# Optimization experiments

Hardware: AMD Instinct MI355X
Metric: run time of the kernel (lower is better)

Reference implementation:

```python
import jax, jax.numpy as jnp
import numpy as np

N_UE = 16384
N_AP = 128
E = 2097152
D = 32

relu = jax.nn.relu


def setup_inputs():
    key = jax.random.key(0)
    ks = jax.random.split(key, 24)
    def g(i, shape, s=0.1):
        return jax.random.normal(ks[i], shape, dtype=jnp.float32) * s
    inp = {}
    inp["x_ue"] = jax.random.uniform(ks[0], (N_UE, 1), dtype=jnp.float32)
    inp["e_ua"] = g(1, (E, 2), 1.0)
    inp["e_au"] = g(2, (E, 2), 1.0)
    inp["src"] = jax.random.randint(ks[3], (E,), 0, N_UE)
    inp["dst"] = jax.random.randint(ks[4], (E,), 0, N_AP)
    # layer 1 (Ue2Ap): ue feat dim 1, ap feat dim 0, edge dim 2
    inp["Wm1_ua"] = g(5, (1 + 2, D)); inp["bm1_ua"] = jnp.zeros((D,), jnp.float32)
    inp["Wm1_au"] = g(6, (2, D));     inp["bm1_au"] = jnp.zeros((D,), jnp.float32)
    inp["Wu1_ap"] = g(7, (D, D));     inp["bu1_ap"] = jnp.zeros((D,), jnp.float32)
    inp["Wu1_ue"] = g(8, (1 + D, D)); inp["bu1_ue"] = jnp.zeros((D,), jnp.float32)
    inp["We1_ua"] = g(9, (2 * D + 2, 2));  inp["be1_ua"] = jnp.zeros((2,), jnp.float32)
    inp["We1_au"] = g(10, (2 * D + 2, 2)); inp["be1_au"] = jnp.zeros((2,), jnp.float32)
    # layers 2-4 stacked (all 32 -> 32)
    inp["Wm_ua"] = g(11, (3, D + 2, D)); inp["bm_ua"] = jnp.zeros((3, D), jnp.float32)
    inp["Wm_au"] = g(12, (3, D + 2, D)); inp["bm_au"] = jnp.zeros((3, D), jnp.float32)
    inp["Wu_ap"] = g(13, (3, 2 * D, D)); inp["bu_ap"] = jnp.zeros((3, D), jnp.float32)
    inp["Wu_ue"] = g(14, (3, 2 * D, D)); inp["bu_ue"] = jnp.zeros((3, D), jnp.float32)
    inp["We_ua"] = g(15, (3, 2 * D + 2, 2)); inp["be_ua"] = jnp.zeros((3, 2), jnp.float32)
    inp["We_au"] = g(16, (3, 2 * D + 2, 2)); inp["be_au"] = jnp.zeros((3, 2), jnp.float32)
    # power head: mlp([32,16]) + Lin(16,1) + Sigmoid
    inp["Wp1"] = g(17, (D, 16)); inp["bp1"] = jnp.zeros((16,), jnp.float32)
    inp["Wp2"] = g(18, (16, 1)); inp["bp2"] = jnp.zeros((1,), jnp.float32)
    return inp


def _het_conv(x_ue, x_ap, e_ua, e_au, src, dst,
              Wm_ua, bm_ua, Wm_au, bm_au,
              Wu_ap, bu_ap, Wu_ue, bu_ue,
              We_ua, be_ua, We_au, be_au):
    # ue -> ap: gather src ue feats + edge attr, MLP, scatter-add to ap
    f_ua = jnp.concatenate([x_ue[src], e_ua], axis=1)        # [E, d_ue+2]
    m_ua = relu(f_ua @ Wm_ua + bm_ua)                        # [E, D]
    agg_ap = jax.ops.segment_sum(m_ua, dst, num_segments=N_AP)
    # ap -> ue: ap has no features in layer 1 (dim 0)
    f_au = e_au if x_ap is None else jnp.concatenate([x_ap[dst], e_au], axis=1)
    m_au = relu(f_au @ Wm_au + bm_au)                        # [E, D]
    agg_ue = jax.ops.segment_sum(m_au, src, num_segments=N_UE)
    # node updates
    h_ap = agg_ap if x_ap is None else jnp.concatenate([x_ap, agg_ap], axis=1)
    x_ap_new = relu(h_ap @ Wu_ap + bu_ap)                    # [N_AP, D]
    x_ue_new = relu(jnp.concatenate([x_ue, agg_ue], axis=1) @ Wu_ue + bu_ue)  # [N_UE, D]
    # edge updates (keep edge_dim = 2)
    pair = jnp.concatenate([x_ue_new[src], x_ap_new[dst]], axis=1)  # [E, 2D]
    e_ua_new = relu(jnp.concatenate([pair, e_ua], axis=1) @ We_ua + be_ua)
    e_au_new = relu(jnp.concatenate([pair, e_au], axis=1) @ We_au + be_au)
    return x_ue_new, x_ap_new, e_ua_new, e_au_new


def reference(x_ue, e_ua, e_au, src, dst,
              Wm1_ua, bm1_ua, Wm1_au, bm1_au, Wu1_ap, bu1_ap, Wu1_ue, bu1_ue,
              We1_ua, be1_ua, We1_au, be1_au,
              Wm_ua, bm_ua, Wm_au, bm_au, Wu_ap, bu_ap, Wu_ue, bu_ue,
              We_ua, be_ua, We_au, be_au,
              Wp1, bp1, Wp2, bp2):
    x_ue, x_ap, e_ua, e_au = _het_conv(
        x_ue, None, e_ua, e_au, src, dst,
        Wm1_ua, bm1_ua, Wm1_au, bm1_au, Wu1_ap, bu1_ap, Wu1_ue, bu1_ue,
        We1_ua, be1_ua, We1_au, be1_au)
    for l in range(3):  # conv2, conv3, conv4
        x_ue, x_ap, e_ua, e_au = _het_conv(
            x_ue, x_ap, e_ua, e_au, src, dst,
            Wm_ua[l], bm_ua[l], Wm_au[l], bm_au[l],
            Wu_ap[l], bu_ap[l], Wu_ue[l], bu_ue[l],
            We_ua[l], be_ua[l], We_au[l], be_au[l])
    power = jax.nn.sigmoid(relu(x_ue @ Wp1 + bp1) @ Wp2 + bp2)  # [N_UE, 1]
    ue_out = jnp.concatenate([x_ue[:, :1], power], axis=1)      # [N_UE, 2]
    return ue_out, x_ap, e_ua, e_au
```

## Files before the change

### kernel.cpp

```cpp
#include <hip/hip_runtime.h>
#include <math.h>

#define N_UE 16384
#define N_AP 128
#define NE   2097152
#define NSB  256
#define EPSB (NE / NSB)
#define APCH 128
#define NPART (N_AP * APCH)

__global__ __launch_bounds__(256) void init_kernel(
    const float* __restrict__ x_ue, const float* __restrict__ Wm1_ua,
    const float* __restrict__ bm1_ua, const float* __restrict__ bm1_au,
    float* __restrict__ Qua, float* __restrict__ Pau)
{
    int i = blockIdx.x * 256 + threadIdx.x;
    int d = i & 31;
    Qua[i] = fmaf(x_ue[i >> 5], Wm1_ua[d], bm1_ua[d]);
    if (i < N_AP * 32) Pau[i] = bm1_au[d];
}

__global__ __launch_bounds__(256) void hist_src(
    const int* __restrict__ src, int* __restrict__ histS)
{
    __shared__ int h[N_UE];
    for (int i = threadIdx.x; i < N_UE; i += 256) h[i] = 0;
    __syncthreads();
    const int beg = blockIdx.x * EPSB;
    for (int e = beg + threadIdx.x; e < beg + EPSB; e += 256)
        atomicAdd(&h[src[e]], 1);
    __syncthreads();
    for (int i = threadIdx.x; i < N_UE; i += 256) histS[blockIdx.x * N_UE + i] = h[i];
}

__global__ __launch_bounds__(256) void colscan_kernel(
    const int* __restrict__ histS, int* __restrict__ baseS, int* __restrict__ cnt)
{
    const int u = blockIdx.x * 256 + threadIdx.x;
    int run = 0;
    for (int b = 0; b < NSB; ++b) {
        int t = histS[b * N_UE + u];
        baseS[b * N_UE + u] = run;
        run += t;
    }
    cnt[u] = run;
}

__global__ __launch_bounds__(256) void scan_kernel(
    const int* __restrict__ cnt, int* __restrict__ offs)
{
    __shared__ int ps[256];
    __shared__ int ps2[257];
    const int t = threadIdx.x;
    const int b0 = t * (N_UE / 256);
    int s = 0;
    for (int i = 0; i < N_UE / 256; ++i) s += cnt[b0 + i];
    ps[t] = s;
    __syncthreads();
    if (t == 0) {
        int r = 0;
        for (int i = 0; i < 256; ++i) { ps2[i] = r; r += ps[i]; }
        ps2[256] = r;
    }
    __syncthreads();
    int r = ps2[t];
    for (int i = 0; i < N_UE / 256; ++i) { offs[b0 + i] = r; r += cnt[b0 + i]; }
    if (t == 255) offs[N_UE] = ps2[256];
}

__global__ __launch_bounds__(256) void scatter_src(
    const int* __restrict__ src, const int* __restrict__ dst,
    const float2* __restrict__ e0au,
    const int* __restrict__ baseS, const int* __restrict__ offs,
    int* __restrict__ dtS, float2* __restrict__ attS, int* __restrict__ invS)
{
    __shared__ int cursor[N_UE];
    const int b = blockIdx.x;
    for (int i = threadIdx.x; i < N_UE; i += 256)
        cursor[i] = offs[i] + baseS[b * N_UE + i];
    __syncthreads();
    const int beg = b * EPSB;
    for (int e = beg + threadIdx.x; e < beg + EPSB; e += 256) {
        int s = src[e];
        int pos = atomicAdd(&cursor[s], 1);
        dtS[pos] = dst[e];
        attS[pos] = e0au[e];
        invS[e] = pos;
    }
}

__global__ __launch_bounds__(256) void hist_dst(
    const int* __restrict__ dst, int* __restrict__ histD)
{
    __shared__ int h[N_AP];
    if (threadIdx.x < N_AP) h[threadIdx.x] = 0;
    __syncthreads();
    const int beg = blockIdx.x * EPSB;
    for (int e = beg + threadIdx.x; e < beg + EPSB; e += 256)
        atomicAdd(&h[dst[e]], 1);
    __syncthreads();
    if (threadIdx.x < N_AP) histD[blockIdx.x * N_AP + threadIdx.x] = h[threadIdx.x];
}

__global__ __launch_bounds__(128) void scan_dst(
    const int* __restrict__ histD, int* __restrict__ offsD, int* __restrict__ offsDnode)
{
    __shared__ int colTot[N_AP], colStart[N_AP];
    const int a = threadIdx.x;
    int run = 0;
    for (int b = 0; b < NSB; ++b) {
        offsD[b * N_AP + a] = run;
        run += histD[b * N_AP + a];
    }
    colTot[a] = run;
    __syncthreads();
    if (a == 0) {
        int r = 0;
        for (int i = 0; i < N_AP; ++i) { colStart[i] = r; r += colTot[i]; }
    }
    __syncthreads();
    const int st = colStart[a];
    offsDnode[a] = st;
    if (a == 0) offsDnode[N_AP] = NE;
    for (int b = 0; b < NSB; ++b) offsD[b * N_AP + a] += st;
}

__global__ __launch_bounds__(256) void scatter_dst(
    const int* __restrict__ src, const int* __restrict__ dst,
    const float2* __restrict__ e0ua, const int* __restrict__ offsD,
    int* __restrict__ srcD, float2* __restrict__ attD, int* __restrict__ invD)
{
    __shared__ int cursor[N_AP];
    const int b = blockIdx.x;
    if (threadIdx.x < N_AP) cursor[threadIdx.x] = offsD[b * N_AP + threadIdx.x];
    __syncthreads();
    const int beg = b * EPSB;
    for (int e = beg + threadIdx.x; e < beg + EPSB; e += 256) {
        int dt = dst[e];
        int pos = atomicAdd(&cursor[dt], 1);
        srcD[pos] = src[e];
        attD[pos] = e0ua[e];
        invD[e] = pos;
    }
}

template<bool EUPD>
__global__ __launch_bounds__(256) void ue_pass(
    const int* __restrict__ offs, const int* __restrict__ dtS,
    const float2* __restrict__ attIn, float2* __restrict__ attOut,
    const float2* __restrict__ RueB, const float2* __restrict__ RapB,
    const float* __restrict__ EcB,
    const float* __restrict__ Pau, const float* __restrict__ cw,
    float* __restrict__ agg_ue)
{
    const int tid = threadIdx.x;
    const int u   = blockIdx.x * 8 + (tid >> 5);
    const int dim = tid & 31;

    const float w0 = cw[dim], w1 = cw[32 + dim];
    float d00 = 0.f, d01 = 0.f, d10 = 0.f, d11 = 0.f, rbx = 0.f, rby = 0.f;
    if constexpr (EUPD) {
        d00 = EcB[0]; d01 = EcB[1]; d10 = EcB[2]; d11 = EcB[3];
        float2 r = RueB[u]; rbx = r.x; rby = r.y;
    }

    const int e0 = offs[u], e1 = offs[u + 1];
    float acc = 0.f;
    #pragma unroll 4
    for (int e = e0; e < e1; ++e) {
        int dt = dtS[e];
        float2 ea = attIn[e];
        if constexpr (EUPD) {
            float2 rp = RapB[dt];
            float m0 = fmaxf(rbx + rp.x + ea.x * d00 + ea.y * d10, 0.f);
            float m1 = fmaxf(rby + rp.y + ea.x * d01 + ea.y * d11, 0.f);
            ea = make_float2(m0, m1);
            if (dim == 0) attOut[e] = ea;
        }
        float p = Pau[dt * 32 + dim];
        acc += fmaxf(fmaf(ea.x, w0, fmaf(ea.y, w1, p)), 0.f);
    }
    agg_ue[u * 32 + dim] = acc;
}

template<bool EUPD>
__global__ __launch_bounds__(256) void ap_pass(
    const int* __restrict__ offsDnode, const int* __restrict__ srcD,
    const float2* __restrict__ attIn, float2* __restrict__ attOut,
    const float2* __restrict__ RueA, const float2* __restrict__ RapA,
    const float* __restrict__ EcA,
    const float* __restrict__ Qua, const float* __restrict__ cu,
    float* __restrict__ partial)
{
    const int tid = threadIdx.x;
    const int gid = blockIdx.x * 8 + (tid >> 5);
    const int dim = tid & 31;
    const int a   = gid >> 7;
    const int c   = gid & 127;

    const float u0 = cu[dim], u1 = cu[32 + dim];
    float c00 = 0.f, c01 = 0.f, c10 = 0.f, c11 = 0.f, rax = 0.f, ray = 0.f;
    if constexpr (EUPD) {
        c00 = EcA[0]; c01 = EcA[1]; c10 = EcA[2]; c11 = EcA[3];
        float2 r = RapA[a]; rax = r.x; ray = r.y;
    }

    const int s0 = offsDnode[a], s1 = offsDnode[a + 1];
    const int len = s1 - s0;
    const int b0 = s0 + (int)(((long long)len * c) >> 7);
    const int b1 = s0 + (int)(((long long)len * (c + 1)) >> 7);

    float acc = 0.f;
    #pragma unroll 4
    for (int e = b0; e < b1; ++e) {
        int s = srcD[e];
        float2 ea = attIn[e];
        if constexpr (EUPD) {
            float2 ru = RueA[s];
            float n0 = fmaxf(rax + ru.x + ea.x * c00 + ea.y * c10, 0.f);
            float n1 = fmaxf(ray + ru.y + ea.x * c01 + ea.y * c11, 0.f);
            ea = make_float2(n0, n1);
            if (dim == 0) attOut[e] = ea;
        }
        float q = Qua[s * 32 + dim];
        acc += fmaxf(fmaf(ea.x, u0, fmaf(ea.y, u1, q)), 0.f);
    }
    partial[gid * 32 + dim] = acc;
}

__global__ __launch_bounds__(256) void final_edge(
    const int* __restrict__ src, const int* __restrict__ dst,
    const int* __restrict__ invS, const int* __restrict__ invD,
    const float2* __restrict__ attS, const float2* __restrict__ attD,
    const float2* __restrict__ RueA, const float2* __restrict__ RueB,
    const float2* __restrict__ RapA, const float2* __restrict__ RapB,
    const float* __restrict__ EcA, const float* __restrict__ EcB,
    float2* __restrict__ out_eua, float2* __restrict__ out_eau)
{
    const int e = blockIdx.x * 256 + threadIdx.x;
    const int s = src[e], dt = dst[e];
    float c00 = EcA[0], c01 = EcA[1], c10 = EcA[2], c11 = EcA[3];
    float d00 = EcB[0], d01 = EcB[1], d10 = EcB[2], d11 = EcB[3];
    float2 eua = attD[invD[e]];
    float2 eau = attS[invS[e]];
    float2 rA = RueA[s], pA = RapA[dt];
    float n0 = fmaxf(rA.x + pA.x + eua.x * c00 + eua.y * c10, 0.f);
    float n1 = fmaxf(rA.y + pA.y + eua.x * c01 + eua.y * c11, 0.f);
    float2 rB = RueB[s], pB = RapB[dt];
    float m0 = fmaxf(rB.x + pB.x + eau.x * d00 + eau.y * d10, 0.f);
    float m1 = fmaxf(rB.y + pB.y + eau.x * d01 + eau.y * d11, 0.f);
    out_eua[e] = make_float2(n0, n1);
    out_eau[e] = make_float2(m0, m1);
}

template<bool FIRST, bool LAST>
__global__ __launch_bounds__(256) void node_ue_kernel(
    const float* __restrict__ x_prev, const float* __restrict__ agg_ue,
    const float* __restrict__ Wu, const float* __restrict__ bu,
    const float* __restrict__ Wm_next, const float* __restrict__ bm_next,
    const float* __restrict__ WeUa, const float* __restrict__ WeUb,
    const float* __restrict__ Wp1, const float* __restrict__ bp1,
    const float* __restrict__ Wp2, const float* __restrict__ bp2,
    float* __restrict__ x_new, float* __restrict__ Qua_next,
    float2* __restrict__ RueA, float2* __restrict__ RueB,
    float2* __restrict__ ue_out)
{
    constexpr int KIN = FIRST ? 33 : 64;
    __shared__ float Wu_s[64 * 32];
    __shared__ float Wm_s[32 * 32];
    __shared__ float WeA_s[64], WeB_s[64];
    __shared__ float bu_s[32], bm_s[32];
    __shared__ float Wp1_s[32 * 16], bp1_s[16], Wp2_s[16];

    const int tid = threadIdx.x;
    for (int i = tid; i < KIN * 32; i += 256) Wu_s[i] = Wu[i];
    if (tid < 32) bu_s[tid] = bu[tid];
    if (!LAST) {
        for (int i = tid; i < 1024; i += 256) Wm_s[i] = Wm_next[i];
        if (tid < 32) bm_s[tid] = bm_next[tid];
    }
    if (tid < 64) { WeA_s[tid] = WeUa[tid]; WeB_s[tid] = WeUb[tid]; }
    if (LAST) {
        for (int i = tid; i < 512; i += 256) Wp1_s[i] = Wp1[i];
        if (tid < 16) { bp1_s[tid] = bp1[tid]; Wp2_s[tid] = Wp2[tid]; }
    }
    __syncthreads();

    const int u = blockIdx.x * 256 + tid;
    float in[KIN];
    if (FIRST) {
        in[0] = x_prev[u];
        #pragma unroll
        for (int k = 0; k < 32; ++k) in[1 + k] = agg_ue[u * 32 + k];
    } else {
        #pragma unroll
        for (int k = 0; k < 32; ++k) in[k] = x_prev[u * 32 + k];
        #pragma unroll
        for (int k = 0; k < 32; ++k) in[32 + k] = agg_ue[u * 32 + k];
    }
    float out[32];
    #pragma unroll
    for (int d = 0; d < 32; ++d) {
        float acc = bu_s[d];
        #pragma unroll
        for (int k = 0; k < KIN; ++k) acc = fmaf(in[k], Wu_s[k * 32 + d], acc);
        out[d] = fmaxf(acc, 0.f);
    }
    #pragma unroll
    for (int d = 0; d < 32; ++d) x_new[u * 32 + d] = out[d];
    if (!LAST) {
        #pragma unroll
        for (int d = 0; d < 32; ++d) {
            float acc = bm_s[d];
            #pragma unroll
            for (int k = 0; k < 32; ++k) acc = fmaf(out[k], Wm_s[k * 32 + d], acc);
            Qua_next[u * 32 + d] = acc;
        }
    }
    float r0 = 0.f, r1 = 0.f, s0 = 0.f, s1 = 0.f;
    #pragma unroll
    for (int k = 0; k < 32; ++k) {
        r0 = fmaf(out[k], WeA_s[k * 2],     r0);
        r1 = fmaf(out[k], WeA_s[k * 2 + 1], r1);
        s0 = fmaf(out[k], WeB_s[k * 2],     s0);
        s1 = fmaf(out[k], WeB_s[k * 2 + 1], s1);
    }
    RueA[u] = make_float2(r0, r1);
    RueB[u] = make_float2(s0, s1);
    if (LAST) {
        float z = bp2[0];
        #pragma unroll
        for (int j = 0; j < 16; ++j) {
            float h = bp1_s[j];
            #pragma unroll
            for (int k = 0; k < 32; ++k) h = fmaf(out[k], Wp1_s[k * 16 + j], h);
            z = fmaf(fmaxf(h, 0.f), Wp2_s[j], z);
        }
        float pw = 1.f / (1.f + expf(-z));
        ue_out[u] = make_float2(out[0], pw);
    }
}

template<bool FIRST, bool LAST>
__global__ __launch_bounds__(256) void node_ap_kernel(
    const float* __restrict__ partial,
    const float* __restrict__ x_prev,
    const float* __restrict__ Wu, const float* __restrict__ bu,
    const float* __restrict__ Wm_next, const float* __restrict__ bm_next,
    const float* __restrict__ WeA, const float* __restrict__ beA,
    const float* __restrict__ WeB, const float* __restrict__ beB,
    float* __restrict__ x_new, float* __restrict__ Pau_next,
    float2* __restrict__ RapA, float2* __restrict__ RapB)
{
    __shared__ float red[256];
    __shared__ float agg_s[32];
    __shared__ float xnew_s[32];
    const int a = blockIdx.x, tid = threadIdx.x;
    const int d = tid & 31, p0 = tid >> 5;
    float acc = 0.f;
    for (int p = p0; p < APCH; p += 8)
        acc += partial[(size_t)(a * APCH + p) * 32 + d];
    red[tid] = acc;
    __syncthreads();
    if (tid < 32) {
        float s = 0.f;
        #pragma unroll
        for (int i = 0; i < 8; ++i) s += red[i * 32 + tid];
        agg_s[tid] = s;
    }
    __syncthreads();
    if (tid < 32) {
        float acc2 = bu[d];
        if (FIRST) {
            #pragma unroll
            for (int k = 0; k < 32; ++k) acc2 = fmaf(agg_s[k], Wu[k * 32 + d], acc2);
        } else {
            #pragma unroll
            for (int k = 0; k < 32; ++k) acc2 = fmaf(x_prev[a * 32 + k], Wu[k * 32 + d], acc2);
            #pragma unroll
            for (int k = 0; k < 32; ++k) acc2 = fmaf(agg_s[k], Wu[(32 + k) * 32 + d], acc2);
        }
        float xn = fmaxf(acc2, 0.f);
        xnew_s[d] = xn;
        x_new[a * 32 + d] = xn;
    }
    __syncthreads();
    if (!LAST) {
        if (tid < 32) {
            float acc3 = bm_next[d];
            #pragma unroll
            for (int k = 0; k < 32; ++k) acc3 = fmaf(xnew_s[k], Wm_next[k * 32 + d], acc3);
            Pau_next[a * 32 + d] = acc3;
        }
    }
    if (tid == 0) {
        float q0 = beA[0], q1 = beA[1], t0 = beB[0], t1 = beB[1];
        #pragma unroll
        for (int k = 0; k < 32; ++k) {
            q0 = fmaf(xnew_s[k], WeA[k * 2],     q0);
            q1 = fmaf(xnew_s[k], WeA[k * 2 + 1], q1);
            t0 = fmaf(xnew_s[k], WeB[k * 2],     t0);
            t1 = fmaf(xnew_s[k], WeB[k * 2 + 1], t1);
        }
        RapA[a] = make_float2(q0, q1);
        RapB[a] = make_float2(t0, t1);
    }
}

extern "C" void kernel_launch(void* const* d_in, const int* in_sizes, int n_in,
                              void* d_out_v, int out_size, void* d_ws, size_t ws_size,
                              hipStream_t stream)
{
    const float*  x_ue   = (const float*)d_in[0];
    const float2* e0ua   = (const float2*)d_in[1];
    const float2* e0au   = (const float2*)d_in[2];
    const int*    src    = (const int*)d_in[3];
    const int*    dst    = (const int*)d_in[4];
    const float* Wm1_ua = (const float*)d_in[5];
    const float* bm1_ua = (const float*)d_in[6];
    const float* Wm1_au = (const float*)d_in[7];
    const float* bm1_au = (const float*)d_in[8];
    const float* Wu1_ap = (const float*)d_in[9];
    const float* bu1_ap = (const float*)d_in[10];
    const float* Wu1_ue = (const float*)d_in[11];
    const float* bu1_ue = (const float*)d_in[12];
    const float* We1_ua = (const float*)d_in[13];
    const float* be1_ua = (const float*)d_in[14];
    const float* We1_au = (const float*)d_in[15];
    const float* be1_au = (const float*)d_in[16];
    const float* Wm_ua  = (const float*)d_in[17];
    const float* bm_ua  = (const float*)d_in[18];
    const float* Wm_au  = (const float*)d_in[19];
    const float* bm_au  = (const float*)d_in[20];
    const float* Wu_ap  = (const float*)d_in[21];
    const float* bu_ap  = (const float*)d_in[22];
    const float* Wu_ue  = (const float*)d_in[23];
    const float* bu_ue  = (const float*)d_in[24];
    const float* We_ua  = (const float*)d_in[25];
    const float* be_ua  = (const float*)d_in[26];
    const float* We_au  = (const float*)d_in[27];
    const float* be_au  = (const float*)d_in[28];
    const float* Wp1    = (const float*)d_in[29];
    const float* bp1    = (const float*)d_in[30];
    const float* Wp2    = (const float*)d_in[31];
    const float* bp2    = (const float*)d_in[32];

    float*  outp    = (float*)d_out_v;
    float2* out_ue  = (float2*)outp;
    float*  out_ap  = outp + N_UE * 2;
    float2* out_eua = (float2*)(outp + N_UE * 2 + N_AP * 32);
    float2* out_eau = (float2*)(outp + N_UE * 2 + N_AP * 32 + (size_t)NE * 2);

    float* ws = (float*)d_ws;
    float* x_ueA  = ws;          ws += N_UE * 32;
    float* x_ueB  = ws;          ws += N_UE * 32;
    float* x_apA  = ws;          ws += N_AP * 32;
    float* x_apB  = ws;          ws += N_AP * 32;
    float* agg_ue = ws;          ws += N_UE * 32;
    float* Qua    = ws;          ws += N_UE * 32;
    float* Pau    = ws;          ws += N_AP * 32;
    float2* RueA  = (float2*)ws; ws += N_UE * 2;
    float2* RueB  = (float2*)ws; ws += N_UE * 2;
    float2* RapA  = (float2*)ws; ws += N_AP * 2;
    float2* RapB  = (float2*)ws; ws += N_AP * 2;
    float* partial = ws;         ws += (size_t)NPART * 32;
    int* cnt   = (int*)ws;       ws += N_UE;
    int* offs  = (int*)ws;       ws += N_UE + 4;
    int* histD = (int*)ws;       ws += NSB * N_AP;
    int* offsD = (int*)ws;       ws += NSB * N_AP;
    int* offsDnode = (int*)ws;   ws += N_AP + 4;
    int* invS  = (int*)ws;       ws += NE;
    int* invD  = (int*)ws;       ws += NE;
    int* dtS   = (int*)ws;       ws += NE;
    int* srcD  = (int*)ws;       ws += NE;
    float2* attS_A = (float2*)ws; ws += (size_t)NE * 2;
    float2* attS_B = (float2*)ws; ws += (size_t)NE * 2;
    float2* attD_A = (float2*)ws; ws += (size_t)NE * 2;
    float2* attD_B = (float2*)ws; ws += (size_t)NE * 2;
    int* histS = (int*)attS_B;
    int* baseS = (int*)attD_B;

    dim3 blk(256);

    hist_src<<<NSB, blk, 0, stream>>>(src, histS);
    colscan_kernel<<<N_UE / 256, blk, 0, stream>>>(histS, baseS, cnt);
    scan_kernel<<<1, blk, 0, stream>>>(cnt, offs);
    scatter_src<<<NSB, blk, 0, stream>>>(src, dst, e0au, baseS, offs, dtS, attS_A, invS);
    hist_dst<<<NSB, blk, 0, stream>>>(dst, histD);
    scan_dst<<<1, dim3(128), 0, stream>>>(histD, offsD, offsDnode);
    scatter_dst<<<NSB, blk, 0, stream>>>(src, dst, e0ua, offsD, srcD, attD_A, invD);

    init_kernel<<<N_UE * 32 / 256, blk, 0, stream>>>(x_ue, Wm1_ua, bm1_ua, bm1_au, Qua, Pau);

    ue_pass<false><<<N_UE / 8, blk, 0, stream>>>(
        offs, dtS, attS_A, nullptr, nullptr, nullptr, nullptr,
        Pau, Wm1_au, agg_ue);
    ap_pass<false><<<NPART / 8, blk, 0, stream>>>(
        offsDnode, srcD, attD_A, nullptr, nullptr, nullptr, nullptr,
        Qua, Wm1_ua + 32, partial);
    node_ue_kernel<true, false><<<N_UE / 256, blk, 0, stream>>>(
        x_ue, agg_ue, Wu1_ue, bu1_ue, Wm_ua, bm_ua, We1_ua, We1_au,
        nullptr, nullptr, nullptr, nullptr,
        x_ueA, Qua, RueA, RueB, nullptr);
    node_ap_kernel<true, false><<<N_AP, blk, 0, stream>>>(
        partial, nullptr, Wu1_ap, bu1_ap, Wm_au, bm_au,
        We1_ua + 64, be1_ua, We1_au + 64, be1_au,
        x_apA, Pau, RapA, RapB);

    ue_pass<true><<<N_UE / 8, blk, 0, stream>>>(
        offs, dtS, attS_A, attS_B, RueB, RapB, We1_au + 128,
        Pau, Wm_au + 1024, agg_ue);
    ap_pass<true><<<NPART / 8, blk, 0, stream>>>(
        offsDnode, srcD, attD_A, attD_B, RueA, RapA, We1_ua + 128,
        Qua, Wm_ua + 1024, partial);
    node_ue_kernel<false, false><<<N_UE / 256, blk, 0, stream>>>(
        x_ueA, agg_ue, Wu_ue, bu_ue, Wm_ua + 1088, bm_ua + 32, We_ua, We_au,
        nullptr, nullptr, nullptr, nullptr,
        x_ueB, Qua, RueA, RueB, nullptr);
    node_ap_kernel<false, false><<<N_AP, blk, 0, stream>>>(
        partial, x_apA, Wu_ap, bu_ap, Wm_au + 1088, bm_au + 32,
        We_ua + 64, be_ua, We_au + 64, be_au,
        x_apB, Pau, RapA, RapB);

    ue_pass<true><<<N_UE / 8, blk, 0, stream>>>(
        offs, dtS, attS_B, attS_A, RueB, RapB, We_au + 128,
        Pau, Wm_au + 2112, agg_ue);
    ap_pass<true><<<NPART / 8, blk, 0, stream>>>(
        offsDnode, srcD, attD_B, attD_A, RueA, RapA, We_ua + 128,
        Qua, Wm_ua + 2112, partial);
    node_ue_kernel<false, false><<<N_UE / 256, blk, 0, stream>>>(
        x_ueB, agg_ue, Wu_ue + 2048, bu_ue + 32, Wm_ua + 2176, bm_ua + 64,
        We_ua + 132, We_au + 132,
        nullptr, nullptr, nullptr, nullptr,
        x_ueA, Qua, RueA, RueB, nullptr);
    node_ap_kernel<false, false><<<N_AP, blk, 0, stream>>>(
        partial, x_apB, Wu_ap + 2048, bu_ap + 32, Wm_au + 2176, bm_au + 64,
        We_ua + 196, be_ua + 2, We_au + 196, be_au + 2,
        x_apA, Pau, RapA, RapB);

    ue_pass<true><<<N_UE / 8, blk, 0, stream>>>(
        offs, dtS, attS_A, attS_B, RueB, RapB, We_au + 260,
        Pau, Wm_au + 3200, agg_ue);
    ap_pass<true><<<NPART / 8, blk, 0, stream>>>(
        offsDnode, srcD, attD_A, attD_B, RueA, RapA, We_ua + 260,
        Qua, Wm_ua + 3200, partial);
    node_ue_kernel<false, true><<<N_UE / 256, blk, 0, stream>>>(
        x_ueA, agg_ue, Wu_ue + 4096, bu_ue + 64, nullptr, nullptr,
        We_ua + 264, We_au + 264,
        Wp1, bp1, Wp2, bp2,
        x_ueB, nullptr, RueA, RueB, out_ue);
    node_ap_kernel<false, true><<<N_AP, blk, 0, stream>>>(
        partial, x_apA, Wu_ap + 4096, bu_ap + 64, nullptr, nullptr,
        We_ua + 328, be_ua + 4, We_au + 328, be_au + 4,
        out_ap, nullptr, RapA, RapB);

    final_edge<<<NE / 256, blk, 0, stream>>>(
        src, dst, invS, invD, attS_B, attD_B,
        RueA, RueB, RapA, RapB,
        We_ua + 392, We_au + 392, out_eua, out_eau);
}
```

Baseline: 1.106 ms.

## Process edges in padded fixed-size chunks per thread with all 32 dims

Replaces the warp-per-node, lane-per-dimension edge passes with a thread-per-chunk scheme. Each node's edge list is padded to multiples of 8 (UE side) or 16 (AP side), using sentinel indices whose feature rows are -1e30 so the ReLU turns padding into zero. Each thread accumulates all 32 dimensions with float4 loads and writes a per-chunk partial, which a separate reduce kernel (or the AP node kernel) sums per node. Edge attributes are now updated in place rather than ping-ponged between two buffers. This aims to remove load imbalance and redundant per-lane index and attribute loads, at the cost of high register use per thread, extra partial-buffer traffic, and one extra reduction launch per layer.

```diff
diff --git a/kernel.cpp b/kernel.cpp
--- a/kernel.cpp
+++ b/kernel.cpp
@@ -6,8 +6,26 @@
 #define NE   2097152
 #define NSB  256
 #define EPSB (NE / NSB)
-#define APCH 128
-#define NPART (N_AP * APCH)
+#define CHS  8
+#define CHD  16
+#define NEP  (NE + CHS * N_UE)
+#define NCHU (NEP / CHS)
+#define NEPD (NE + CHD * N_AP)
+#define NCHD (NEPD / CHD)
+#define NCHD_AL 131328
+
+#define RFL(x) __int_as_float(__builtin_amdgcn_readfirstlane(__float_as_int(x)))
+
+__global__ __launch_bounds__(256) void prefill(
+    int* __restrict__ dtS, int* __restrict__ srcD,
+    int* __restrict__ cnS, int* __restrict__ cnD)
+{
+    int i = blockIdx.x * 256 + threadIdx.x;
+    dtS[i] = N_AP;
+    if (i < NEPD) srcD[i] = N_UE;
+    if (i < NCHU) cnS[i] = -1;
+    if (i < NCHD_AL) cnD[i] = -1;
+}
 
 __global__ __launch_bounds__(256) void init_kernel(
     const float* __restrict__ x_ue, const float* __restrict__ Wm1_ua,
@@ -18,6 +36,7 @@
     int d = i & 31;
     Qua[i] = fmaf(x_ue[i >> 5], Wm1_ua[d], bm1_ua[d]);
     if (i < N_AP * 32) Pau[i] = bm1_au[d];
+    if (i < 32) { Qua[N_UE * 32 + i] = -1e30f; Pau[N_AP * 32 + i] = -1e30f; }
 }
 
 __global__ __launch_bounds__(256) void hist_src(
@@ -46,15 +65,15 @@
     cnt[u] = run;
 }
 
-__global__ __launch_bounds__(256) void scan_kernel(
-    const int* __restrict__ cnt, int* __restrict__ offs)
+__global__ __launch_bounds__(256) void scan_src(
+    const int* __restrict__ cnt, int* __restrict__ CU)
 {
     __shared__ int ps[256];
     __shared__ int ps2[257];
     const int t = threadIdx.x;
     const int b0 = t * (N_UE / 256);
     int s = 0;
-    for (int i = 0; i < N_UE / 256; ++i) s += cnt[b0 + i];
+    for (int i = 0; i < N_UE / 256; ++i) s += (cnt[b0 + i] + CHS - 1) / CHS;
     ps[t] = s;
     __syncthreads();
     if (t == 0) {
@@ -64,20 +83,20 @@
     }
     __syncthreads();
     int r = ps2[t];
-    for (int i = 0; i < N_UE / 256; ++i) { offs[b0 + i] = r; r += cnt[b0 + i]; }
-    if (t == 255) offs[N_UE] = ps2[256];
+    for (int i = 0; i < N_UE / 256; ++i) { CU[b0 + i] = r; r += (cnt[b0 + i] + CHS - 1) / CHS; }
+    if (t == 255) CU[N_UE] = ps2[256];
 }
 
 __global__ __launch_bounds__(256) void scatter_src(
     const int* __restrict__ src, const int* __restrict__ dst,
     const float2* __restrict__ e0au,
-    const int* __restrict__ baseS, const int* __restrict__ offs,
+    const int* __restrict__ baseS, const int* __restrict__ CU,
     int* __restrict__ dtS, float2* __restrict__ attS, int* __restrict__ invS)
 {
     __shared__ int cursor[N_UE];
     const int b = blockIdx.x;
     for (int i = threadIdx.x; i < N_UE; i += 256)
-        cursor[i] = offs[i] + baseS[b * N_UE + i];
+        cursor[i] = CU[i] * CHS + baseS[b * N_UE + i];
     __syncthreads();
     const int beg = b * EPSB;
     for (int e = beg + threadIdx.x; e < beg + EPSB; e += 256) {
@@ -103,7 +122,7 @@
 }
 
 __global__ __launch_bounds__(128) void scan_dst(
-    const int* __restrict__ histD, int* __restrict__ offsD, int* __restrict__ offsDnode)
+    const int* __restrict__ histD, int* __restrict__ offsD, int* __restrict__ CA)
 {
     __shared__ int colTot[N_AP], colStart[N_AP];
     const int a = threadIdx.x;
@@ -116,12 +135,15 @@
     __syncthreads();
     if (a == 0) {
         int r = 0;
-        for (int i = 0; i < N_AP; ++i) { colStart[i] = r; r += colTot[i]; }
+        for (int i = 0; i < N_AP; ++i) {
+            CA[i] = r;
+            colStart[i] = r * CHD;
+            r += (colTot[i] + CHD - 1) / CHD;
+        }
+        CA[N_AP] = r;
     }
     __syncthreads();
     const int st = colStart[a];
-    offsDnode[a] = st;
-    if (a == 0) offsDnode[N_AP] = NE;
     for (int b = 0; b < NSB; ++b) offsD[b * N_AP + a] += st;
 }
 
@@ -144,88 +166,134 @@
     }
 }
 
+__global__ __launch_bounds__(256) void build_map_src(
+    const int* __restrict__ CU, int* __restrict__ cnS)
+{
+    const int u = blockIdx.x * 256 + threadIdx.x;
+    const int c0 = CU[u], c1 = CU[u + 1];
+    for (int c = c0; c < c1; ++c) cnS[c] = u;
+}
+
+__global__ __launch_bounds__(128) void build_map_dst(
+    const int* __restrict__ CA, int* __restrict__ cnD)
+{
+    const int a = threadIdx.x;
+    const int c0 = CA[a], c1 = CA[a + 1];
+    for (int c = c0; c < c1; ++c) cnD[c] = a;
+}
+
 template<bool EUPD>
-__global__ __launch_bounds__(256) void ue_pass(
-    const int* __restrict__ offs, const int* __restrict__ dtS,
-    const float2* __restrict__ attIn, float2* __restrict__ attOut,
+__global__ __launch_bounds__(256) void pass_src(
+    const int* __restrict__ cnS, const int* __restrict__ dtS,
+    float2* __restrict__ attS,
     const float2* __restrict__ RueB, const float2* __restrict__ RapB,
     const float* __restrict__ EcB,
     const float* __restrict__ Pau, const float* __restrict__ cw,
-    float* __restrict__ agg_ue)
-{
-    const int tid = threadIdx.x;
-    const int u   = blockIdx.x * 8 + (tid >> 5);
-    const int dim = tid & 31;
-
-    const float w0 = cw[dim], w1 = cw[32 + dim];
+    float* __restrict__ partialU)
+{
+    const int ch = blockIdx.x * 256 + threadIdx.x;
+    const int u = cnS[ch];
+    if (u < 0) return;
+    float w0v[32], w1v[32];
+    #pragma unroll
+    for (int d = 0; d < 32; ++d) { w0v[d] = RFL(cw[d]); w1v[d] = RFL(cw[32 + d]); }
     float d00 = 0.f, d01 = 0.f, d10 = 0.f, d11 = 0.f, rbx = 0.f, rby = 0.f;
     if constexpr (EUPD) {
-        d00 = EcB[0]; d01 = EcB[1]; d10 = EcB[2]; d11 = EcB[3];
+        d00 = RFL(EcB[0]); d01 = RFL(EcB[1]); d10 = RFL(EcB[2]); d11 = RFL(EcB[3]);
         float2 r = RueB[u]; rbx = r.x; rby = r.y;
     }
-
-    const int e0 = offs[u], e1 = offs[u + 1];
-    float acc = 0.f;
-    #pragma unroll 4
-    for (int e = e0; e < e1; ++e) {
-        int dt = dtS[e];
-        float2 ea = attIn[e];
+    const float4* __restrict__ Pau4 = (const float4*)Pau;
+    const int base = ch * CHS;
+    float4 acc[8];
+    #pragma unroll
+    for (int q = 0; q < 8; ++q) acc[q] = make_float4(0.f, 0.f, 0.f, 0.f);
+    #pragma unroll
+    for (int j = 0; j < CHS; ++j) {
+        int dt = dtS[base + j];
+        float2 a = attS[base + j];
         if constexpr (EUPD) {
             float2 rp = RapB[dt];
-            float m0 = fmaxf(rbx + rp.x + ea.x * d00 + ea.y * d10, 0.f);
-            float m1 = fmaxf(rby + rp.y + ea.x * d01 + ea.y * d11, 0.f);
-            ea = make_float2(m0, m1);
-            if (dim == 0) attOut[e] = ea;
-        }
-        float p = Pau[dt * 32 + dim];
-        acc += fmaxf(fmaf(ea.x, w0, fmaf(ea.y, w1, p)), 0.f);
-    }
-    agg_ue[u * 32 + dim] = acc;
+            float m0 = fmaxf(rbx + rp.x + a.x * d00 + a.y * d10, 0.f);
+            float m1 = fmaxf(rby + rp.y + a.x * d01 + a.y * d11, 0.f);
+            a = make_float2(m0, m1);
+            attS[base + j] = a;
+        }
+        const float4* pr = Pau4 + dt * 8;
+        #pragma unroll
+        for (int q = 0; q < 8; ++q) {
+            float4 pv = pr[q];
+            acc[q].x += fmaxf(fmaf(a.x, w0v[q*4+0], fmaf(a.y, w1v[q*4+0], pv.x)), 0.f);
+            acc[q].y += fmaxf(fmaf(a.x, w0v[q*4+1], fmaf(a.y, w1v[q*4+1], pv.y)), 0.f);
+            acc[q].z += fmaxf(fmaf(a.x, w0v[q*4+2], fmaf(a.y, w1v[q*4+2], pv.z)), 0.f);
+            acc[q].w += fmaxf(fmaf(a.x, w0v[q*4+3], fmaf(a.y, w1v[q*4+3], pv.w)), 0.f);
+        }
+    }
+    float4* pu = (float4*)(partialU + (size_t)ch * 32);
+    #pragma unroll
+    for (int q = 0; q < 8; ++q) pu[q] = acc[q];
 }
 
 template<bool EUPD>
-__global__ __launch_bounds__(256) void ap_pass(
-    const int* __restrict__ offsDnode, const int* __restrict__ srcD,
-    const float2* __restrict__ attIn, float2* __restrict__ attOut,
+__global__ __launch_bounds__(256) void pass_dst(
+    const int* __restrict__ cnD, const int* __restrict__ srcD,
+    float2* __restrict__ attD,
     const float2* __restrict__ RueA, const float2* __restrict__ RapA,
     const float* __restrict__ EcA,
     const float* __restrict__ Qua, const float* __restrict__ cu,
-    float* __restrict__ partial)
-{
-    const int tid = threadIdx.x;
-    const int gid = blockIdx.x * 8 + (tid >> 5);
-    const int dim = tid & 31;
-    const int a   = gid >> 7;
-    const int c   = gid & 127;
-
-    const float u0 = cu[dim], u1 = cu[32 + dim];
+    float* __restrict__ partialA)
+{
+    const int ch = blockIdx.x * 256 + threadIdx.x;
+    const int a = cnD[ch];
+    if (a < 0) return;
+    float u0v[32], u1v[32];
+    #pragma unroll
+    for (int d = 0; d < 32; ++d) { u0v[d] = RFL(cu[d]); u1v[d] = RFL(cu[32 + d]); }
     float c00 = 0.f, c01 = 0.f, c10 = 0.f, c11 = 0.f, rax = 0.f, ray = 0.f;
     if constexpr (EUPD) {
-        c00 = EcA[0]; c01 = EcA[1]; c10 = EcA[2]; c11 = EcA[3];
+        c00 = RFL(EcA[0]); c01 = RFL(EcA[1]); c10 = RFL(EcA[2]); c11 = RFL(EcA[3]);
         float2 r = RapA[a]; rax = r.x; ray = r.y;
     }
-
-    const int s0 = offsDnode[a], s1 = offsDnode[a + 1];
-    const int len = s1 - s0;
-    const int b0 = s0 + (int)(((long long)len * c) >> 7);
-    const int b1 = s0 + (int)(((long long)len * (c + 1)) >> 7);
-
-    float acc = 0.f;
+    const float4* __restrict__ Qua4 = (const float4*)Qua;
+    const int base = ch * CHD;
+    float4 acc[8];
+    #pragma unroll
+    for (int q = 0; q < 8; ++q) acc[q] = make_float4(0.f, 0.f, 0.f, 0.f);
     #pragma unroll 4
-    for (int e = b0; e < b1; ++e) {
-        int s = srcD[e];
-        float2 ea = attIn[e];
+    for (int j = 0; j < CHD; ++j) {
+        int s = srcD[base + j];
+        float2 a2 = attD[base + j];
         if constexpr (EUPD) {
             float2 ru = RueA[s];
-            float n0 = fmaxf(rax + ru.x + ea.x * c00 + ea.y * c10, 0.f);
-            float n1 = fmaxf(ray + ru.y + ea.x * c01 + ea.y * c11, 0.f);
-            ea = make_float2(n0, n1);
-            if (dim == 0) attOut[e] = ea;
-        }
-        float q = Qua[s * 32 + dim];
-        acc += fmaxf(fmaf(ea.x, u0, fmaf(ea.y, u1, q)), 0.f);
-    }
-    partial[gid * 32 + dim] = acc;
+            float n0 = fmaxf(rax + ru.x + a2.x * c00 + a2.y * c10, 0.f);
+            float n1 = fmaxf(ray + ru.y + a2.x * c01 + a2.y * c11, 0.f);
+            a2 = make_float2(n0, n1);
+            attD[base + j] = a2;
+        }
+        const float4* qr = Qua4 + s * 8;
+        #pragma unroll
+        for (int q = 0; q < 8; ++q) {
+            float4 qv = qr[q];
+            acc[q].x += fmaxf(fmaf(a2.x, u0v[q*4+0], fmaf(a2.y, u1v[q*4+0], qv.x)), 0.f);
+            acc[q].y += fmaxf(fmaf(a2.x, u0v[q*4+1], fmaf(a2.y, u1v[q*4+1], qv.y)), 0.f);
+            acc[q].z += fmaxf(fmaf(a2.x, u0v[q*4+2], fmaf(a2.y, u1v[q*4+2], qv.z)), 0.f);
+            acc[q].w += fmaxf(fmaf(a2.x, u0v[q*4+3], fmaf(a2.y, u1v[q*4+3], qv.w)), 0.f);
+        }
+    }
+    float4* pa = (float4*)(partialA + (size_t)ch * 32);
+    #pragma unroll
+    for (int q = 0; q < 8; ++q) pa[q] = acc[q];
+}
+
+__global__ __launch_bounds__(256) void reduce_ue(
+    const int* __restrict__ CU, const float* __restrict__ partialU,
+    float* __restrict__ agg_ue)
+{
+    const int g   = (blockIdx.x * 256 + threadIdx.x) >> 5;
+    const int dim = threadIdx.x & 31;
+    const int c0 = CU[g], c1 = CU[g + 1];
+    float acc = 0.f;
+    for (int c = c0; c < c1; ++c) acc += partialU[(size_t)c * 32 + dim];
+    agg_ue[g * 32 + dim] = acc;
 }
 
 __global__ __launch_bounds__(256) void final_edge(
@@ -343,7 +411,7 @@
 
 template<bool FIRST, bool LAST>
 __global__ __launch_bounds__(256) void node_ap_kernel(
-    const float* __restrict__ partial,
+    const float* __restrict__ partialA, const int* __restrict__ CA,
     const float* __restrict__ x_prev,
     const float* __restrict__ Wu, const float* __restrict__ bu,
     const float* __restrict__ Wm_next, const float* __restrict__ bm_next,
@@ -357,9 +425,10 @@
     __shared__ float xnew_s[32];
     const int a = blockIdx.x, tid = threadIdx.x;
     const int d = tid & 31, p0 = tid >> 5;
+    const int c0 = CA[a], c1 = CA[a + 1];
     float acc = 0.f;
-    for (int p = p0; p < APCH; p += 8)
-        acc += partial[(size_t)(a * APCH + p) * 32 + d];
+    for (int p = c0 + p0; p < c1; p += 8)
+        acc += partialA[(size_t)p * 32 + d];
     red[tid] = acc;
     __syncthreads();
     if (tid < 32) {
@@ -457,105 +526,105 @@
     float* x_apA  = ws;          ws += N_AP * 32;
     float* x_apB  = ws;          ws += N_AP * 32;
     float* agg_ue = ws;          ws += N_UE * 32;
-    float* Qua    = ws;          ws += N_UE * 32;
-    float* Pau    = ws;          ws += N_AP * 32;
-    float2* RueA  = (float2*)ws; ws += N_UE * 2;
-    float2* RueB  = (float2*)ws; ws += N_UE * 2;
-    float2* RapA  = (float2*)ws; ws += N_AP * 2;
-    float2* RapB  = (float2*)ws; ws += N_AP * 2;
-    float* partial = ws;         ws += (size_t)NPART * 32;
+    float* Qua    = ws;          ws += (N_UE + 1) * 32;
+    float* Pau    = ws;          ws += (N_AP + 1) * 32;
+    float2* RueA  = (float2*)ws; ws += (N_UE + 2) * 2;
+    float2* RueB  = (float2*)ws; ws += (N_UE + 2) * 2;
+    float2* RapA  = (float2*)ws; ws += (N_AP + 2) * 2;
+    float2* RapB  = (float2*)ws; ws += (N_AP + 2) * 2;
     int* cnt   = (int*)ws;       ws += N_UE;
-    int* offs  = (int*)ws;       ws += N_UE + 4;
+    int* CU    = (int*)ws;       ws += N_UE + 4;
     int* histD = (int*)ws;       ws += NSB * N_AP;
     int* offsD = (int*)ws;       ws += NSB * N_AP;
-    int* offsDnode = (int*)ws;   ws += N_AP + 4;
+    int* CA    = (int*)ws;       ws += N_AP + 4;
+    int* cnS   = (int*)ws;       ws += NCHU;
+    int* cnD   = (int*)ws;       ws += NCHD_AL;
     int* invS  = (int*)ws;       ws += NE;
     int* invD  = (int*)ws;       ws += NE;
-    int* dtS   = (int*)ws;       ws += NE;
-    int* srcD  = (int*)ws;       ws += NE;
-    float2* attS_A = (float2*)ws; ws += (size_t)NE * 2;
-    float2* attS_B = (float2*)ws; ws += (size_t)NE * 2;
-    float2* attD_A = (float2*)ws; ws += (size_t)NE * 2;
-    float2* attD_B = (float2*)ws; ws += (size_t)NE * 2;
-    int* histS = (int*)attS_B;
-    int* baseS = (int*)attD_B;
+    int* dtS   = (int*)ws;       ws += NEP;
+    int* srcD  = (int*)ws;       ws += NEPD;
+    float2* attS = (float2*)ws;  ws += (size_t)NEP * 2;
+    float2* attD = (float2*)ws;  ws += (size_t)NEPD * 2;
+    float* partialU = ws;        ws += (size_t)NCHU * 32;
+    float* partialA = ws;        ws += (size_t)NCHD_AL * 32;
+    int* histS = (int*)partialU;
+    int* baseS = (int*)(partialU + (size_t)NSB * N_UE);
 
     dim3 blk(256);
 
+    prefill<<<NEP / 256, blk, 0, stream>>>(dtS, srcD, cnS, cnD);
     hist_src<<<NSB, blk, 0, stream>>>(src, histS);
     colscan_kernel<<<N_UE / 256, blk, 0, stream>>>(histS, baseS, cnt);
-    scan_kernel<<<1, blk, 0, stream>>>(cnt, offs);
-    scatter_src<<<NSB, blk, 0, stream>>>(src, dst, e0au, baseS, offs, dtS, attS_A, invS);
+    scan_src<<<1, blk, 0, stream>>>(cnt, CU);
+    scatter_src<<<NSB, blk, 0, stream>>>(src, dst, e0au, baseS, CU, dtS, attS, invS);
     hist_dst<<<NSB, blk, 0, stream>>>(dst, histD);
-    scan_dst<<<1, dim3(128), 0, stream>>>(histD, offsD, offsDnode);
-    scatter_dst<<<NSB, blk, 0, stream>>>(src, dst, e0ua, offsD, srcD, attD_A, invD);
+    scan_dst<<<1, dim3(128), 0, stream>>>(histD, offsD, CA);
+    scatter_dst<<<NSB, blk, 0, stream>>>(src, dst, e0ua, offsD, srcD, attD, invD);
+    build_map_src<<<N_UE / 256, blk, 0, stream>>>(CU, cnS);
+    build_map_dst<<<1, dim3(128), 0, stream>>>(CA, cnD);
 
     init_kernel<<<N_UE * 32 / 256, blk, 0, stream>>>(x_ue, Wm1_ua, bm1_ua, bm1_au, Qua, Pau);
 
-    ue_pass<false><<<N_UE / 8, blk, 0, stream>>>(
-        offs, dtS, attS_A, nullptr, nullptr, nullptr, nullptr,
-        Pau, Wm1_au, agg_ue);
-    ap_pass<false><<<NPART / 8, blk, 0, stream>>>(
-        offsDnode, srcD, attD_A, nullptr, nullptr, nullptr, nullptr,
-        Qua, Wm1_ua + 32, partial);
+    pass_src<false><<<NCHU / 256, blk, 0, stream>>>(
+        cnS, dtS, attS, nullptr, nullptr, nullptr, Pau, Wm1_au, partialU);
+    pass_dst<false><<<NCHD_AL / 256, blk, 0, stream>>>(
+        cnD, srcD, attD, nullptr, nullptr, nullptr, Qua, Wm1_ua + 32, partialA);
+    reduce_ue<<<N_UE * 32 / 256, blk, 0, stream>>>(CU, partialU, agg_ue);
     node_ue_kernel<true, false><<<N_UE / 256, blk, 0, stream>>>(
         x_ue, agg_ue, Wu1_ue, bu1_ue, Wm_ua, bm_ua, We1_ua, We1_au,
         nullptr, nullptr, nullptr, nullptr,
         x_ueA, Qua, RueA, RueB, nullptr);
     node_ap_kernel<true, false><<<N_AP, blk, 0, stream>>>(
-        partial, nullptr, Wu1_ap, bu1_ap, Wm_au, bm_au,
+        partialA, CA, nullptr, Wu1_ap, bu1_ap, Wm_au, bm_au,
         We1_ua + 64, be1_ua, We1_au + 64, be1_au,
         x_apA, Pau, RapA, RapB);
 
-    ue_pass<true><<<N_UE / 8, blk, 0, stream>>>(
-        offs, dtS, attS_A, attS_B, RueB, RapB, We1_au + 128,
-        Pau, Wm_au + 1024, agg_ue);
-    ap_pass<true><<<NPART / 8, blk, 0, stream>>>(
-        offsDnode, srcD, attD_A, attD_B, RueA, RapA, We1_ua + 128,
-        Qua, Wm_ua + 1024, partial);
+    pass_src<true><<<NCHU / 256, blk, 0, stream>>>(
+        cnS, dtS, attS, RueB, RapB, We1_au + 128, Pau, Wm_au + 1024, partialU);
+    pass_dst<true><<<NCHD_AL / 256, blk, 0, stream>>>(
+        cnD, srcD, attD, RueA, RapA, We1_ua + 128, Qua, Wm_ua + 1024, partialA);
+    reduce_ue<<<N_UE * 32 / 256, blk, 0, stream>>>(CU, partialU, agg_ue);
     node_ue_kernel<false, false><<<N_UE / 256, blk, 0, stream>>>(
         x_ueA, agg_ue, Wu_ue, bu_ue, Wm_ua + 1088, bm_ua + 32, We_ua, We_au,
         nullptr, nullptr, nullptr, nullptr,
         x_ueB, Qua, RueA, RueB, nullptr);
     node_ap_kernel<false, false><<<N_AP, blk, 0, stream>>>(
-        partial, x_apA, Wu_ap, bu_ap, Wm_au + 1088, bm_au + 32,
+        partialA, CA, x_apA, Wu_ap, bu_ap, Wm_au + 1088, bm_au + 32,
         We_ua + 64, be_ua, We_au + 64, be_au,
         x_apB, Pau, RapA, RapB);
 
-    ue_pass<true><<<N_UE / 8, blk, 0, stream>>>(
-        offs, dtS, attS_B, attS_A, RueB, RapB, We_au + 128,
-        Pau, Wm_au + 2112, agg_ue);
-    ap_pass<true><<<NPART / 8, blk, 0, stream>>>(
-        offsDnode, srcD, attD_B, attD_A, RueA, RapA, We_ua + 128,
-        Qua, Wm_ua + 2112, partial);
+    pass_src<true><<<NCHU / 256, blk, 0, stream>>>(
+        cnS, dtS, attS, RueB, RapB, We_au + 128, Pau, Wm_au + 2112, partialU);
+    pass_dst<true><<<NCHD_AL / 256, blk, 0, stream>>>(
+        cnD, srcD, attD, RueA, RapA, We_ua + 128, Qua, Wm_ua + 2112, partialA);
+    reduce_ue<<<N_UE * 32 / 256, blk, 0, stream>>>(CU, partialU, agg_ue);
     node_ue_kernel<false, false><<<N_UE / 256, blk, 0, stream>>>(
         x_ueB, agg_ue, Wu_ue + 2048, bu_ue + 32, Wm_ua + 2176, bm_ua + 64,
         We_ua + 132, We_au + 132,
         nullptr, nullptr, nullptr, nullptr,
         x_ueA, Qua, RueA, RueB, nullptr);
     node_ap_kernel<false, false><<<N_AP, blk, 0, stream>>>(
-        partial, x_apB, Wu_ap + 2048, bu_ap + 32, Wm_au + 2176, bm_au + 64,
+        partialA, CA, x_apB, Wu_ap + 2048, bu_ap + 32, Wm_au + 2176, bm_au + 64,
         We_ua + 196, be_ua + 2, We_au + 196, be_au + 2,
         x_apA, Pau, RapA, RapB);
 
-    ue_pass<true><<<N_UE / 8, blk, 0, stream>>>(
-        offs, dtS, attS_A, attS_B, RueB, RapB, We_au + 260,
-        Pau, Wm_au + 3200, agg_ue);
-    ap_pass<true><<<NPART / 8, blk, 0, stream>>>(
-        offsDnode, srcD, attD_A, attD_B, RueA, RapA, We_ua + 260,
-        Qua, Wm_ua + 3200, partial);
+    pass_src<true><<<NCHU / 256, blk, 0, stream>>>(
+        cnS, dtS, attS, RueB, RapB, We_au + 260, Pau, Wm_au + 3200, partialU);
+    pass_dst<true><<<NCHD_AL / 256, blk, 0, stream>>>(
+        cnD, srcD, attD, RueA, RapA, We_ua + 260, Qua, Wm_ua + 3200, partialA);
+    reduce_ue<<<N_UE * 32 / 256, blk, 0, stream>>>(CU, partialU, agg_ue);
     node_ue_kernel<false, true><<<N_UE / 256, blk, 0, stream>>>(
         x_ueA, agg_ue, Wu_ue + 4096, bu_ue + 64, nullptr, nullptr,
         We_ua + 264, We_au + 264,
         Wp1, bp1, Wp2, bp2,
         x_ueB, nullptr, RueA, RueB, out_ue);
     node_ap_kernel<false, true><<<N_AP, blk, 0, stream>>>(
-        partial, x_apA, Wu_ap + 4096, bu_ap + 64, nullptr, nullptr,
+        partialA, CA, x_apA, Wu_ap + 4096, bu_ap + 64, nullptr, nullptr,
         We_ua + 328, be_ua + 4, We_au + 328, be_au + 4,
         out_ap, nullptr, RapA, RapB);
 
     final_edge<<<NE / 256, blk, 0, stream>>>(
-        src, dst, invS, invD, attS_B, attD_B,
+        src, dst, invS, invD, attS, attD,
         RueA, RueB, RapA, RapB,
         We_ua + 392, We_au + 392, out_eua, out_eau);
 }
```

New measurement: 996.4 us. 9.9% less time.
